# Performance work log

Measured on AMD Instinct MI355X. Metric: run time of the kernel, lower is better.

## Reference

```python
import jax, jax.numpy as jnp
import numpy as np

BLADES = ['', '1', '2', '3', '12', '13', '23', '123']
GEO = (3, 0, 0)  # geometrical_def: 3 basis vectors squaring to +1
NB = 8  # multivector_length

def _sq(idx):
    if idx < GEO[0] + 1:
        return 1
    if idx < GEO[0] + GEO[1] + 1:
        return -1
    return 0

def _ga_mul(a, b):
    l1 = [int(c) for c in a]; l2 = [int(c) for c in b]
    s = 1; i1 = 0; i2 = 0; n = len(l1); out = []
    while i1 < len(l1) and i2 < len(l2):
        if l1[i1] == l2[i2]:
            if (n - 1) % 2 != 0:
                s = -s
            s *= _sq(l1[i1]); n -= 1; i1 += 1; i2 += 1
        elif l1[i1] > l2[i2]:
            if n % 2 != 0:
                s = -s
            out.append(l2[i2]); i2 += 1
        else:
            out.append(l1[i1]); n -= 1; i1 += 1
    out += l1[i1:] + l2[i2:]
    return s, ''.join(map(str, out))

def cayley_table():
    # T[i, j, k] = s such that blade_i * blade_j = s * blade_k
    T = np.zeros((NB, NB, NB), dtype=np.float32)
    for i in range(NB):
        for j in range(NB):
            s, idx = _ga_mul(BLADES[i], BLADES[j])
            T[i, j, BLADES.index(idx)] = s
    return jnp.asarray(T)

_CAYLEY = cayley_table()

def setup_inputs() -> dict:
    key = jax.random.key(0)
    k1, k2, k3 = jax.random.split(key, 3)
    BS, C_IN, UNITS = 512, 1024, 1024
    x = jax.random.normal(k1, (NB * BS, C_IN), dtype=jnp.float32)
    W = jax.random.normal(k2, (C_IN, NB * UNITS), dtype=jnp.float32) * (1.0 / np.sqrt(C_IN))
    bias = jax.random.normal(k3, (1, NB * UNITS), dtype=jnp.float32) * 0.02
    return {"input_tensor": x, "W": W, "bias": bias}

def reference(input_tensor, W, bias):
    M = input_tensor.shape[0] // NB   # per-blade batch size
    U = W.shape[1] // NB              # per-blade output channels
    y = input_tensor @ W              # (8M, 8U) dense linear op
    y = y.reshape(NB, M, NB * U)      # split along batch axis into blades i
    y = y.at[0].add(bias[0])          # BiasLayer applied to blade-0 split only
    y = y.reshape(NB, M, NB, U)       # split along channel axis into blades j
    # fused Cayley combine: out[k] = sum_{i,j} T[i,j,k] * y[i,:,j,:]
    out = jnp.einsum('imju,ijk->kmu', y, _CAYLEY)
    return out.reshape(NB * M, U)
```

## Files before the change

kernel.cpp:

```cpp
#include <hip/hip_runtime.h>
#include <stdint.h>

#define NBL 8
#define MBS 512
#define CIN 1024
#define UQ  1024

__device__ __constant__ int   px_sA[4] = {0,1,4,2};
__device__ __constant__ int   px_sB[4] = {3,5,7,6};
__device__ __constant__ int   px_vA[4] = {0,1,4,5};
__device__ __constant__ float px_cA0[4] = {1,1,1,-1};
__device__ __constant__ float px_cA1[4] = {1,-1,1,1};
__device__ __constant__ int   px_vB[4] = {3,2,7,6};
__device__ __constant__ float px_cB0[4] = {1,1,-1,1};
__device__ __constant__ float px_cB1[4] = {-1,1,1,1};
__device__ __constant__ int c_sa[8][4] = {
  {0,8,1,9},{0,4,1,5},{0,8,1,9},{0,4,1,5},
  {2,10,3,11},{2,6,3,7},{2,10,3,11},{2,6,3,7}};
__device__ __constant__ int c_sb[8][4] = {
  {0,4,2,6},{4,0,6,2},{1,5,3,7},{5,1,7,3},
  {0,4,2,6},{4,0,6,2},{1,5,3,7},{5,1,7,3}};
__device__ __constant__ int   c_eb0[8] = {0,4,1,2,1,2,0,4};
__device__ __constant__ float c_es0[8] = {1,1,1,-1,1,1,1,-1};
__device__ __constant__ int   c_eb1[8] = {3,7,5,6,5,6,3,7};
__device__ __constant__ float c_es1[8] = {1,1,-1,1,1,1,-1,1};

__device__ __constant__ int c_sigma[8][8] = {
  {0,1,2,3,4,5,6,7},{1,0,4,5,2,3,7,6},{2,4,0,6,1,7,3,5},{3,5,6,0,7,1,2,4},
  {4,2,1,7,0,6,5,3},{5,3,7,1,6,0,4,2},{6,7,3,2,5,4,0,1},{7,6,5,4,3,2,1,0}};
__device__ __constant__ int c_sg[8][8] = {
  {1,1,1,1,1,1,1,1},{1,1,1,1,1,1,1,1},{1,-1,1,1,-1,-1,1,-1},{1,-1,-1,1,1,-1,-1,1},
  {-1,1,-1,-1,1,1,-1,1},{-1,1,1,-1,-1,1,1,-1},{-1,-1,1,-1,1,-1,1,1},{-1,-1,1,-1,1,-1,1,1}};

typedef short bf16x8 __attribute__((ext_vector_type(8)));
typedef float f32x4 __attribute__((ext_vector_type(4)));

__device__ __forceinline__ uint32_t f2bf(float f) {
  uint32_t u = __float_as_uint(f);
  return (u + 0x7fffu + ((u >> 16) & 1u)) >> 16;
}
__device__ __forceinline__ uint32_t pk2(float lo, float hi) {
  return f2bf(lo) | (f2bf(hi) << 16);
}

__global__ void cvt_x_kernel(const float* __restrict__ x, uint4* __restrict__ xv) {
  __shared__ uint4 tA[32 * 33], tB[32 * 33];
  const int tid = threadIdx.x;
  const int tx = tid & 31, ty = tid >> 5;
  const int p  = blockIdx.x >> 2;
  const int cb = blockIdx.x & 3;
  const int m0 = blockIdx.y * 32;
  const int sA = px_sA[p] * MBS, sB = px_sB[p] * MBS;
  const float cA0 = px_cA0[p], cA1 = px_cA1[p];
  const float cB0 = px_cB0[p], cB1 = px_cB1[p];
#pragma unroll
  for (int r = 0; r < 4; ++r) {
    const int m = m0 + ty + r * 8;
    const float* pa = x + (size_t)(sA + m) * CIN + cb * 256 + tx * 8;
    const float* pb = x + (size_t)(sB + m) * CIN + cb * 256 + tx * 8;
    float4 a0 = *(const float4*)pa, a1 = *(const float4*)(pa + 4);
    float4 b0 = *(const float4*)pb, b1 = *(const float4*)(pb + 4);
    uint4 vA, vB;
    vA.x = pk2(cA0*a0.x + cA1*b0.x, cA0*a0.y + cA1*b0.y);
    vA.y = pk2(cA0*a0.z + cA1*b0.z, cA0*a0.w + cA1*b0.w);
    vA.z = pk2(cA0*a1.x + cA1*b1.x, cA0*a1.y + cA1*b1.y);
    vA.w = pk2(cA0*a1.z + cA1*b1.z, cA0*a1.w + cA1*b1.w);
    vB.x = pk2(cB0*a0.x + cB1*b0.x, cB0*a0.y + cB1*b0.y);
    vB.y = pk2(cB0*a0.z + cB1*b0.z, cB0*a0.w + cB1*b0.w);
    vB.z = pk2(cB0*a1.x + cB1*b1.x, cB0*a1.y + cB1*b1.y);
    vB.w = pk2(cB0*a1.z + cB1*b1.z, cB0*a1.w + cB1*b1.w);
    tA[tx * 33 + ty + r * 8] = vA;
    tB[tx * 33 + ty + r * 8] = vB;
  }
  __syncthreads();
  const int vA = px_vA[p], vB = px_vB[p];
#pragma unroll
  for (int ph = 0; ph < 4; ++ph) {
    const int slot = ph * 256 + tid;
    const int cc = slot >> 5, mm = slot & 31;
    const size_t off = (size_t)(cb * 32 + cc) * 512 + m0 + mm;
    uint4 a = tA[cc * 33 + mm];
    uint4 b = tB[cc * 33 + mm];
    xv[(size_t)vA * 65536 + off] = a;
    xv[(size_t)vB * 65536 + off] = b;
    if (p >= 2) {
      uint4 na, nb;
      na.x = a.x ^ 0x80008000u; na.y = a.y ^ 0x80008000u;
      na.z = a.z ^ 0x80008000u; na.w = a.w ^ 0x80008000u;
      nb.x = b.x ^ 0x80008000u; nb.y = b.y ^ 0x80008000u;
      nb.z = b.z ^ 0x80008000u; nb.w = b.w ^ 0x80008000u;
      xv[(size_t)(vA + 4) * 65536 + off] = na;
      xv[(size_t)(vB + 4) * 65536 + off] = nb;
    }
  }
}

__global__ void cvt_w_kernel(const float* __restrict__ w, uint4* __restrict__ wv) {
  __shared__ float ta[32][65], tb[32][65];
  const int tid = threadIdx.x;
  const int tx = tid & 63, ty = tid >> 6;
  const int p  = blockIdx.x >> 4;
  const int nb = blockIdx.x & 15;
  const int k0 = blockIdx.y * 32;
  const int sAc = px_sA[p] * UQ + nb * 64;
  const int sBc = px_sB[p] * UQ + nb * 64;
#pragma unroll
  for (int r = 0; r < 8; ++r) {
    const int kr = ty * 8 + r;
    ta[kr][tx] = w[(size_t)(k0 + kr) * 8192 + sAc + tx];
    tb[kr][tx] = w[(size_t)(k0 + kr) * 8192 + sBc + tx];
  }
  __syncthreads();
  {
    const int cc = tid >> 6;
    const int uu = tid & 63;
    const float cA0 = 0.5f * px_cA0[p], cA1 = 0.5f * px_cA1[p];
    const float cB0 = 0.5f * px_cB0[p], cB1 = 0.5f * px_cB1[p];
    float eA[8], eB[8];
#pragma unroll
    for (int q = 0; q < 8; ++q) {
      const float a = ta[cc * 8 + q][uu], b = tb[cc * 8 + q][uu];
      eA[q] = cA0 * a + cA1 * b;
      eB[q] = cB0 * a + cB1 * b;
    }
    uint4 oA, oB;
    oA.x = pk2(eA[0], eA[1]); oA.y = pk2(eA[2], eA[3]);
    oA.z = pk2(eA[4], eA[5]); oA.w = pk2(eA[6], eA[7]);
    oB.x = pk2(eB[0], eB[1]); oB.y = pk2(eB[2], eB[3]);
    oB.z = pk2(eB[4], eB[5]); oB.w = pk2(eB[6], eB[7]);
    const size_t off = (size_t)(blockIdx.y * 4 + cc) * 1024 + nb * 64 + uu;
    wv[(size_t)px_vA[p] * 131072 + off] = oA;
    wv[(size_t)px_vB[p] * 131072 + off] = oB;
  }
}

__global__ void bias_fill(const float* __restrict__ bias, float4* __restrict__ out) {
  int idx = blockIdx.x * 256 + threadIdx.x;
  int row = idx >> 8;
  int c4 = idx & 255;
  int k = row >> 9;
  out[idx] = ((const float4*)(bias + k * UQ))[c4];
}

__global__ void merge_kernel(float* out, const float* __restrict__ part,
                             const float* __restrict__ bias) {
  const int q4 = blockIdx.x * 256 + threadIdx.x;
  f32x4* o4 = (f32x4*)out;
  const f32x4* p4 = (const f32x4*)part;
  const f32x4* b4 = (const f32x4*)bias;
  f32x4 P[8];
#pragma unroll
  for (int d = 0; d < 8; ++d)
    P[d] = o4[d * 131072 + q4] + p4[d * 131072 + q4];
  const int u4 = q4 & 255;
  o4[0 * 131072 + q4] = P[0] + P[6] + b4[0 * 256 + u4];
  o4[1 * 131072 + q4] = P[2] + P[4] + b4[1 * 256 + u4];
  o4[2 * 131072 + q4] = P[5] - P[3] + b4[2 * 256 + u4];
  o4[3 * 131072 + q4] = P[0] - P[6] + b4[3 * 256 + u4];
  o4[4 * 131072 + q4] = P[1] - P[7] + b4[4 * 256 + u4];
  o4[5 * 131072 + q4] = P[4] - P[2] + b4[5 * 256 + u4];
  o4[6 * 131072 + q4] = P[3] + P[5] + b4[6 * 256 + u4];
  o4[7 * 131072 + q4] = P[1] + P[7] + b4[7 * 256 + u4];
}

#define BAR() do { asm volatile("s_barrier" ::: "memory");                    \
                   __builtin_amdgcn_sched_barrier(0); } while (0)
#define VMW(N) asm volatile("s_waitcnt vmcnt(" #N ")" ::: "memory")

template<int ATOMIC>
__global__ __launch_bounds__(256, 2) void ga_cplx(
    const uint16_t* __restrict__ xv, const uint16_t* __restrict__ wv,
    float* __restrict__ out, float* __restrict__ part) {
  __shared__ uint16_t lds[4][8192];

  const int tid  = threadIdx.x;
  const int bid  = blockIdx.x;
  const int s    = bid >> 8;
  const int d    = (bid >> 5) & 7;
  const int mt   = (bid >> 3) & 3;
  const int ut   = bid & 7;
  const int lane = tid & 63;
  const int wid  = tid >> 6;
  const int wr   = wid >> 1, wc = wid & 1;
  const int r15  = lane & 15, hi = lane >> 4;

  const uint16_t* aB0 = xv + (size_t)c_sa[d][s * 2 + 0] * 524288;
  const uint16_t* aB1 = xv + (size_t)c_sa[d][s * 2 + 1] * 524288;
  const uint16_t* bB0 = wv + (size_t)c_sb[d][s * 2 + 0] * 1048576;
  const uint16_t* bB1 = wv + (size_t)c_sb[d][s * 2 + 1] * 1048576;

  const int hc = tid >> 7;
  const size_t mrow8 = (size_t)(mt * 128 + (tid & 127)) * 8;
  const size_t urow8 = (size_t)(ut * 128 + (tid & 127)) * 8;

  f32x4 acc[4][4];
  const f32x4 z = {0.f, 0.f, 0.f, 0.f};
#pragma unroll
  for (int a = 0; a < 4; ++a)
#pragma unroll
    for (int b = 0; b < 4; ++b) acc[a][b] = z;

  auto stage = [&](int u) {
    const uint16_t* pa = (u & 32) ? aB1 : aB0;
    const uint16_t* pb = (u & 32) ? bB1 : bB0;
    const int c0 = (u & 31) << 2;
    uint16_t* la = lds[u & 3];
    uint16_t* lb = lds[u & 3] + 4096;
#pragma unroll
    for (int u2 = 0; u2 < 2; ++u2) {
      const int cc = c0 + u2 * 2 + hc;
      __builtin_amdgcn_global_load_lds(
          (const __attribute__((address_space(1))) uint32_t*)(pa + (size_t)cc * 4096 + mrow8),
          (__attribute__((address_space(3))) uint32_t*)(la + (u2 * 256 + tid) * 8), 16, 0, 0);
      __builtin_amdgcn_global_load_lds(
          (const __attribute__((address_space(1))) uint32_t*)(pb + (size_t)cc * 8192 + urow8),
          (__attribute__((address_space(3))) uint32_t*)(lb + (u2 * 256 + tid) * 8), 16, 0, 0);
    }
  };

#define READF(FA, FB, RB) {                                                   \
  const uint16_t* b_ = lds[(RB)];                                             \
  _Pragma("unroll")                                                           \
  for (int f = 0; f < 4; ++f)                                                 \
    FA[f] = *(const bf16x8*)(b_ + ((hi << 7) + wr * 64 + f * 16 + r15) * 8);  \
  _Pragma("unroll")                                                           \
  for (int g = 0; g < 4; ++g)                                                 \
    FB[g] = *(const bf16x8*)(b_ + 4096 + ((hi << 7) + wc * 64 + g * 16 + r15) * 8); \
}

#define KEEP(FA, FB)                                                          \
  asm volatile("" : "+v"(FA[0]), "+v"(FA[1]), "+v"(FA[2]), "+v"(FA[3]),       \
                    "+v"(FB[0]), "+v"(FB[1]), "+v"(FB[2]), "+v"(FB[3]));

#define MFMA16(CA, CB) {                                                      \
  _Pragma("unroll")                                                           \
  for (int f = 0; f < 4; ++f)                                                 \
    _Pragma("unroll")                                                         \
    for (int g = 0; g < 4; ++g)                                               \
      acc[f][g] = __builtin_amdgcn_mfma_f32_16x16x32_bf16(                    \
          CA[f], CB[g], acc[f][g], 0, 0, 0);                                  \
}

#define ITER(T, CA, CB, LA, LB) {                                             \
  VMW(4);                                                                     \
  BAR();                                                                      \
  stage(((T) + 3 < 63) ? (T) + 3 : 63);                                       \
  READF(LA, LB, ((((T) + 1 < 63) ? (T) + 1 : 63) & 3));                       \
  __builtin_amdgcn_sched_barrier(0);                                          \
  MFMA16(CA, CB);                                                             \
  __builtin_amdgcn_sched_barrier(0);                                          \
  KEEP(LA, LB);                                                               \
}

  bf16x8 fCa[4], fCb[4], fNa[4], fNb[4];

  stage(0); stage(1); stage(2);
  VMW(4);
  BAR();
  READF(fCa, fCb, 0);
  KEEP(fCa, fCb);

  for (int t = 0; t < 64; t += 2) {
    ITER(t,     fCa, fCb, fNa, fNb);
    ITER(t + 1, fNa, fNb, fCa, fCb);
  }

  const int row0 = mt * 128 + wr * 64;
  const int col0 = ut * 128 + wc * 64;
  if constexpr (ATOMIC) {
    const int rb0 = c_eb0[d], rb1 = c_eb1[d];
    const float es0 = c_es0[d], es1 = c_es1[d];
#pragma unroll
    for (int g = 0; g < 4; ++g) {
      const int col = col0 + g * 16 + r15;
#pragma unroll
      for (int f = 0; f < 4; ++f) {
        const int r0 = row0 + f * 16 + hi * 4;
#pragma unroll
        for (int r = 0; r < 4; ++r) {
          const float val = acc[f][g][r];
          unsafeAtomicAdd(&out[(size_t)(rb0 * MBS + r0 + r) * UQ + col], es0 * val);
          unsafeAtomicAdd(&out[(size_t)(rb1 * MBS + r0 + r) * UQ + col], es1 * val);
        }
      }
    }
  } else {
    float* dst = (s ? part : out) + (size_t)d * 524288;
#pragma unroll
    for (int g = 0; g < 4; ++g) {
      const int col = col0 + g * 16 + r15;
#pragma unroll
      for (int f = 0; f < 4; ++f) {
        const int r0 = row0 + f * 16 + hi * 4;
#pragma unroll
        for (int r = 0; r < 4; ++r)
          dst[(size_t)(r0 + r) * UQ + col] = acc[f][g][r];
      }
    }
  }
}

__global__ void ga_naive(const float* __restrict__ x, const float* __restrict__ w,
                         const float* __restrict__ bias, float* __restrict__ out) {
  int col = blockIdx.x * 256 + threadIdx.x;
  int row = blockIdx.y;
  int k = row >> 9, m = row & 511;
  float acc = bias[k * UQ + col];
  for (int i = 0; i < 8; ++i) {
    int j = c_sigma[i][k];
    float s = (float)c_sg[i][k];
    const float* xr = x + (size_t)(i * MBS + m) * CIN;
    const float* wc = w + (size_t)j * UQ + col;
    float a = 0.f;
    for (int c = 0; c < CIN; ++c) a = fmaf(xr[c], wc[(size_t)c * (NBL * UQ)], a);
    acc = fmaf(s, a, acc);
  }
  out[(size_t)row * UQ + col] = acc;
}

extern "C" void kernel_launch(void* const* d_in, const int* in_sizes, int n_in,
                              void* d_out, int out_size, void* d_ws, size_t ws_size,
                              hipStream_t stream) {
  const float* x    = (const float*)d_in[0];
  const float* W    = (const float*)d_in[1];
  const float* bias = (const float*)d_in[2];
  float* out = (float*)d_out;

  const size_t needA = 44u * 1024u * 1024u;
  const size_t needB = 28u * 1024u * 1024u;
  if (ws_size < needB) {
    ga_naive<<<dim3(4, 4096), dim3(256), 0, stream>>>(x, W, bias, out);
    return;
  }

  uint16_t* xv = (uint16_t*)d_ws;
  uint16_t* wv = xv + 6291456;
  float* part  = (float*)((char*)d_ws + 29360128);

  cvt_x_kernel<<<dim3(16, 16), dim3(256), 0, stream>>>(x, (uint4*)xv);
  cvt_w_kernel<<<dim3(64, 32), dim3(256), 0, stream>>>(W, (uint4*)wv);

  if (ws_size >= needA) {
    ga_cplx<0><<<dim3(512), dim3(256), 0, stream>>>(xv, wv, out, part);
    merge_kernel<<<dim3(512), dim3(256), 0, stream>>>(out, part, bias);
  } else {
    bias_fill<<<dim3(4096), dim3(256), 0, stream>>>(bias, (float4*)out);
    ga_cplx<1><<<dim3(512), dim3(256), 0, stream>>>(xv, wv, out, nullptr);
  }
}
```

Baseline: 64.11 us.

## Add four-way K-split GEMM with larger tiles and four-partial merge kernel

Adds a new GEMM kernel that divides the work into four K-slices (s=0..3), each using 256x128 output tiles with 32-deep reductions and a triple-buffered LDS pipeline. Slice 0 writes to out and the other three write to separate partial buffers. A new merge kernel sums the four partials and applies the Cayley combine plus bias. This path runs only when the workspace is large enough. The larger tiles should cut redundant global loads, but they bring extra partial-buffer traffic (three 16MB writes plus reads) and higher register pressure.

```diff
diff --git a/kernel.cpp b/kernel.cpp
--- a/kernel.cpp
+++ b/kernel.cpp
@@ -163,9 +163,122 @@
   o4[7 * 131072 + q4] = P[1] + P[7] + b4[7 * 256 + u4];
 }
 
+__global__ void merge4_kernel(float* out, const float* __restrict__ pt,
+                              const float* __restrict__ bias) {
+  const int q4 = blockIdx.x * 256 + threadIdx.x;
+  f32x4* o4 = (f32x4*)out;
+  const f32x4* p1 = (const f32x4*)pt;
+  const f32x4* p2 = p1 + 1048576;
+  const f32x4* p3 = p2 + 1048576;
+  const f32x4* b4 = (const f32x4*)bias;
+  f32x4 P[8];
+#pragma unroll
+  for (int d = 0; d < 8; ++d) {
+    const size_t o = (size_t)d * 131072 + q4;
+    P[d] = o4[o] + p1[o] + p2[o] + p3[o];
+  }
+  const int u4 = q4 & 255;
+  o4[0 * 131072 + q4] = P[0] + P[6] + b4[0 * 256 + u4];
+  o4[1 * 131072 + q4] = P[2] + P[4] + b4[1 * 256 + u4];
+  o4[2 * 131072 + q4] = P[5] - P[3] + b4[2 * 256 + u4];
+  o4[3 * 131072 + q4] = P[0] - P[6] + b4[3 * 256 + u4];
+  o4[4 * 131072 + q4] = P[1] - P[7] + b4[4 * 256 + u4];
+  o4[5 * 131072 + q4] = P[4] - P[2] + b4[5 * 256 + u4];
+  o4[6 * 131072 + q4] = P[3] + P[5] + b4[6 * 256 + u4];
+  o4[7 * 131072 + q4] = P[1] + P[7] + b4[7 * 256 + u4];
+}
+
 #define BAR() do { asm volatile("s_barrier" ::: "memory");                    \
                    __builtin_amdgcn_sched_barrier(0); } while (0)
 #define VMW(N) asm volatile("s_waitcnt vmcnt(" #N ")" ::: "memory")
+
+__global__ __launch_bounds__(256, 2) void ga_split4(
+    const uint16_t* __restrict__ xv, const uint16_t* __restrict__ wv,
+    float* __restrict__ out, float* __restrict__ part) {
+  __shared__ uint16_t lds[3][12288];
+
+  const int tid  = threadIdx.x;
+  const int bid  = blockIdx.x;
+  const int s    = bid >> 7;
+  const int d    = (bid >> 4) & 7;
+  const int mt   = (bid >> 3) & 1;
+  const int ut   = bid & 7;
+  const int lane = tid & 63;
+  const int wid  = tid >> 6;
+  const int wr   = wid >> 1, wc = wid & 1;
+  const int r15  = lane & 15, hi = lane >> 4;
+
+  const uint16_t* aB = xv + (size_t)c_sa[d][s] * 524288;
+  const uint16_t* bB = wv + (size_t)c_sb[d][s] * 1048576;
+
+  f32x4 acc[8][4];
+  const f32x4 z = {0.f, 0.f, 0.f, 0.f};
+#pragma unroll
+  for (int a = 0; a < 8; ++a)
+#pragma unroll
+    for (int b = 0; b < 4; ++b) acc[a][b] = z;
+
+  auto stage = [&](int u) {
+    const int c0 = u << 2;
+    uint16_t* la = lds[u % 3];
+    uint16_t* lb = lds[u % 3] + 8192;
+#pragma unroll
+    for (int r = 0; r < 4; ++r) {
+      const int e = r * 256 + tid;
+      __builtin_amdgcn_global_load_lds(
+          (const __attribute__((address_space(1))) uint32_t*)
+              (aB + ((size_t)(c0 + (e >> 8)) * 512 + mt * 256 + (e & 255)) * 8),
+          (__attribute__((address_space(3))) uint32_t*)(la + e * 8), 16, 0, 0);
+    }
+#pragma unroll
+    for (int r = 0; r < 2; ++r) {
+      const int e = r * 256 + tid;
+      __builtin_amdgcn_global_load_lds(
+          (const __attribute__((address_space(1))) uint32_t*)
+              (bB + ((size_t)(c0 + (e >> 7)) * 1024 + ut * 128 + (e & 127)) * 8),
+          (__attribute__((address_space(3))) uint32_t*)(lb + e * 8), 16, 0, 0);
+    }
+  };
+
+  stage(0); stage(1);
+
+  for (int t = 0; t < 32; ++t) {
+    VMW(6);
+    BAR();
+    stage((t + 2 < 32) ? t + 2 : 31);
+    const uint16_t* L = lds[t % 3];
+    bf16x8 af[8], bf[4];
+#pragma unroll
+    for (int f = 0; f < 8; ++f)
+      af[f] = *(const bf16x8*)(L + ((hi << 8) + wr * 128 + f * 16 + r15) * 8);
+#pragma unroll
+    for (int g = 0; g < 4; ++g)
+      bf[g] = *(const bf16x8*)(L + 8192 + ((hi << 7) + wc * 64 + g * 16 + r15) * 8);
+    __builtin_amdgcn_sched_barrier(0);
+#pragma unroll
+    for (int f = 0; f < 8; ++f)
+#pragma unroll
+      for (int g = 0; g < 4; ++g)
+        acc[f][g] = __builtin_amdgcn_mfma_f32_16x16x32_bf16(
+            af[f], bf[g], acc[f][g], 0, 0, 0);
+  }
+
+  float* dst = ((s == 0) ? out : part + (size_t)(s - 1) * 4194304) +
+               (size_t)d * 524288;
+  const int row0 = mt * 256 + wr * 128;
+  const int col0 = ut * 128 + wc * 64;
+#pragma unroll
+  for (int g = 0; g < 4; ++g) {
+    const int col = col0 + g * 16 + r15;
+#pragma unroll
+    for (int f = 0; f < 8; ++f) {
+      const int r0 = row0 + f * 16 + hi * 4;
+#pragma unroll
+      for (int r = 0; r < 4; ++r)
+        dst[(size_t)(r0 + r) * UQ + col] = acc[f][g][r];
+    }
+  }
+}
 
 template<int ATOMIC>
 __global__ __launch_bounds__(256, 2) void ga_cplx(
@@ -326,6 +439,7 @@
   const float* bias = (const float*)d_in[2];
   float* out = (float*)d_out;
 
+  const size_t needC = 79691776u;
   const size_t needA = 44u * 1024u * 1024u;
   const size_t needB = 28u * 1024u * 1024u;
   if (ws_size < needB) {
@@ -340,7 +454,10 @@
   cvt_x_kernel<<<dim3(16, 16), dim3(256), 0, stream>>>(x, (uint4*)xv);
   cvt_w_kernel<<<dim3(64, 32), dim3(256), 0, stream>>>(W, (uint4*)wv);
 
-  if (ws_size >= needA) {
+  if (ws_size >= needC) {
+    ga_split4<<<dim3(512), dim3(256), 0, stream>>>(xv, wv, out, part);
+    merge4_kernel<<<dim3(512), dim3(256), 0, stream>>>(out, part, bias);
+  } else if (ws_size >= needA) {
     ga_cplx<0><<<dim3(512), dim3(256), 0, stream>>>(xv, wv, out, part);
     merge_kernel<<<dim3(512), dim3(256), 0, stream>>>(out, part, bias);
   } else {
```

Result: slower. 73.19 us (+14.2%).
